# Kernel tuning notes

Hardware: AMD Instinct MI355X
Metric: run time of the kernel (lower is better)

Reference implementation:

```python
import jax, jax.numpy as jnp
import numpy as np


def _hardswish(x):
    return x * jnp.clip(x + 3.0, 0.0, 6.0) / 6.0


def _rel_coords_table(W):
    # [1, 2W-1, 2W-1, 2], log-spaced continuous relative coords (SwinV2)
    rc = jnp.arange(-(W - 1), W, dtype=jnp.float32)
    grid = jnp.stack(jnp.meshgrid(rc, rc, indexing='ij'), axis=-1)[None]
    grid = grid / float(W - 1) * 8.0
    return jnp.sign(grid) * jnp.log2(jnp.abs(grid) + 1.0) / np.float32(np.log2(8.0))


def _rel_pos_index(W):
    # [N, N] int indices into the (2W-1)^2 bias table
    coords = np.stack(np.meshgrid(np.arange(W), np.arange(W), indexing='ij')).reshape(2, -1)
    rel = (coords[:, :, None] - coords[:, None, :]).transpose(1, 2, 0)  # [N, N, 2]
    rel[:, :, 0] += W - 1
    rel[:, :, 1] += W - 1
    rel[:, :, 0] *= 2 * W - 1
    return jnp.asarray(rel.sum(-1))


def setup_inputs() -> dict:
    key = jax.random.key(0)
    ks = jax.random.split(key, 6)
    dim, num_heads, W = 512, 16, 8
    N = W * W
    B, nW = 2048, 64
    return {
        'x': jax.random.normal(ks[0], (B, N, dim), jnp.float32),
        'mask': jax.random.normal(ks[1], (nW, N, N), jnp.float32),
        'w_qkv': jax.random.normal(ks[2], (dim, 3 * dim), jnp.float32) * 0.02,
        'w_out': jax.random.normal(ks[3], (dim, dim), jnp.float32) * 0.02,
        'cpb_w1': jax.random.normal(ks[4], (2, 512), jnp.float32) * 0.02,
        'cpb_w2': jax.random.normal(ks[5], (512, num_heads), jnp.float32) * 0.02,
        'logits_scale': jnp.log(10.0 * jnp.ones((num_heads, 1, 1), jnp.float32)),
        'window_size': W,
        'num_heads': num_heads,
    }


def reference(x, mask, w_qkv, w_out, cpb_w1, cpb_w2, logits_scale, window_size, num_heads):
    B, N, C = x.shape
    hd = C // num_heads
    qkv = (x @ w_qkv).reshape(B, N, 3, num_heads, hd).transpose(2, 0, 3, 1, 4)
    q, k, v = qkv[0], qkv[1], qkv[2]  # [B, H, N, hd]

    # cosine attention (L2-normalized q, k) with clamped learned logit scale
    qn = q / jnp.clip(jnp.linalg.norm(q, axis=-1, keepdims=True), 1e-12)
    kn = k / jnp.clip(jnp.linalg.norm(k, axis=-1, keepdims=True), 1e-12)
    attn = jnp.einsum('bhnd,bhmd->bhnm', qn, kn)
    scale = jnp.exp(jnp.minimum(logits_scale, jnp.log(jnp.float32(100.0))))  # [H,1,1]
    attn = attn * scale[None]

    # continuous position bias via tiny MLP + index gather, sigmoid-scaled
    table = _rel_coords_table(window_size)                       # [1, 2W-1, 2W-1, 2]
    bias_table = (_hardswish(table @ cpb_w1) @ cpb_w2).reshape(-1, num_heads)
    idx = _rel_pos_index(window_size)                            # [N, N]
    bias = bias_table[idx.reshape(-1)].reshape(N, N, num_heads).transpose(2, 0, 1)
    attn = attn + 16.0 * jax.nn.sigmoid(bias)[None]

    if mask is not None:
        nW = mask.shape[0]
        attn = attn.reshape(B // nW, nW, num_heads, N, N) + mask[None, :, None]
        attn = attn.reshape(B, num_heads, N, N)

    # NOTE: original uses nn.Softmax(1) -> softmax over the HEAD axis; replicate faithfully
    attn = jax.nn.softmax(attn, axis=1)

    out = jnp.einsum('bhnm,bhmd->bhnd', attn, v).transpose(0, 2, 1, 3).reshape(B, N, C)
    return out @ w_out
```

## Files before the change

kernel.cpp:

```cpp
#include <hip/hip_runtime.h>
#include <hip/hip_bf16.h>

typedef unsigned short u16;
typedef unsigned int u32;
typedef __attribute__((ext_vector_type(8))) short bf16x8;
typedef __attribute__((ext_vector_type(4))) float f32x4;
typedef __attribute__((ext_vector_type(4))) float float4v;

__device__ __forceinline__ float bf2f(u16 v) {
  union { u32 u; float f; } x; x.u = ((u32)v) << 16; return x.f;
}
__device__ __forceinline__ u16 f2bf(float f) {
  union { u32 u; float f; } x; x.f = f;
  return (u16)((x.u + 0x7fffu + ((x.u >> 16) & 1u)) >> 16);
}

__device__ __forceinline__ void gload16(const void* g, void* l) {
  __builtin_amdgcn_global_load_lds(
      (const __attribute__((address_space(1))) u32*)g,
      (__attribute__((address_space(3))) u32*)l, 16, 0, 0);
}

#define MFMA16(a, bfr, cacc) __builtin_amdgcn_mfma_f32_16x16x32_bf16((a), (bfr), (cacc), 0, 0, 0)


__global__ void transpose_kernel(const float* __restrict__ in, u16* __restrict__ out,
                                 int R, int C) {
  int t = blockIdx.x * blockDim.x + threadIdx.x;
  if (t >= R * C) return;
  int c = t / R, r = t % R;
  out[t] = f2bf(in[r * C + c]);
}

__global__ void bias_tab_kernel(const float* __restrict__ w1, const float* __restrict__ w2,
                                float* __restrict__ tab) {
  int t = blockIdx.x * blockDim.x + threadIdx.x;
  if (t >= 225 * 16) return;
  int r = t >> 4, h = t & 15;
  int i = r / 15, j = r % 15;
  float gi = (float)(i - 7) * (8.0f / 7.0f);
  float gj = (float)(j - 7) * (8.0f / 7.0f);
  float si = (gi > 0.f) ? 1.f : ((gi < 0.f) ? -1.f : 0.f);
  float sj = (gj > 0.f) ? 1.f : ((gj < 0.f) ? -1.f : 0.f);
  float t0 = si * log2f(fabsf(gi) + 1.0f) * (1.0f / 3.0f);
  float t1 = sj * log2f(fabsf(gj) + 1.0f) * (1.0f / 3.0f);
  float acc = 0.f;
  for (int k = 0; k < 512; ++k) {
    float a = t0 * w1[k] + t1 * w1[512 + k];
    float hs = a * fminf(fmaxf(a + 3.f, 0.f), 6.f) * (1.f / 6.f);
    acc += hs * w2[k * 16 + h];
  }
  tab[t] = acc;
}

__global__ void bias16_kernel(const float* __restrict__ tab, float* __restrict__ b16) {
  int t = blockIdx.x * blockDim.x + threadIdx.x;
  if (t >= 16 * 64 * 64) return;
  int h = t >> 12, nm = t & 4095, n = nm >> 6, m = nm & 63;
  int idx = ((n >> 3) - (m >> 3) + 7) * 15 + ((n & 7) - (m & 7) + 7);
  float b = tab[idx * 16 + h];
  b16[t] = 16.0f / (1.0f + expf(-b));
}

template <bool F32OUT>
__global__ __launch_bounds__(256) void gemm_bt(const u16* __restrict__ A,
                                               const u16* __restrict__ Bt,
                                               void* __restrict__ Cout,
                                               int M, int N, int K) {
  __shared__ u16 lA[128 * 64];
  __shared__ u16 lB[128 * 64];
  const int tid = threadIdx.x;
  const int w = tid >> 6, l = tid & 63;
  const int lg = l >> 4, li = l & 15;
  const int nbn = N >> 7;
  const int nwg = gridDim.x;
  int bidx = blockIdx.x;
  int q = nwg >> 3, r = nwg & 7;
  int xcd = bidx & 7, pos = bidx >> 3;
  int swz = (xcd < r ? xcd * (q + 1) : r * (q + 1) + (xcd - r) * q) + pos;
  int bm = swz / nbn, bn = swz % nbn;
  const int wr = w >> 1, wc = w & 1;

  f32x4 acc[4][4];
#pragma unroll
  for (int i = 0; i < 4; i++)
#pragma unroll
    for (int j = 0; j < 4; j++) acc[i][j] = (f32x4){0.f, 0.f, 0.f, 0.f};

  const u16* Abase = A + (size_t)(bm * 128) * K;
  const u16* Bbase = Bt + (size_t)(bn * 128) * K;

  for (int k0 = 0; k0 < K; k0 += 64) {
#pragma unroll
    for (int i = 0; i < 4; ++i) {
      int c = w * 256 + i * 64 + l;
      int row = c >> 3, kc = c & 7;
      gload16(Abase + (size_t)row * K + k0 + kc * 8, (u16*)lA + c * 8);
      gload16(Bbase + (size_t)row * K + k0 + kc * 8, (u16*)lB + c * 8);
    }
    __syncthreads();
#pragma unroll
    for (int kk = 0; kk < 2; ++kk) {
      bf16x8 af[4], bfr[4];
#pragma unroll
      for (int t = 0; t < 4; ++t) {
        int row = wr * 64 + t * 16 + li;
        af[t] = *(const bf16x8*)&lA[row * 64 + kk * 32 + lg * 8];
        int col = wc * 64 + t * 16 + li;
        bfr[t] = *(const bf16x8*)&lB[col * 64 + kk * 32 + lg * 8];
      }
#pragma unroll
      for (int tm = 0; tm < 4; ++tm)
#pragma unroll
        for (int tn = 0; tn < 4; ++tn)
          acc[tm][tn] = MFMA16(af[tm], bfr[tn], acc[tm][tn]);
    }
    __syncthreads();
  }
  int r0 = bm * 128 + wr * 64 + lg * 4;
  int c0 = bn * 128 + wc * 64 + li;
#pragma unroll
  for (int tm = 0; tm < 4; ++tm)
#pragma unroll
    for (int tn = 0; tn < 4; ++tn)
#pragma unroll
      for (int j = 0; j < 4; ++j) {
        size_t off = (size_t)(r0 + tm * 16 + j) * N + c0 + tn * 16;
        if (F32OUT)
          ((float*)Cout)[off] = acc[tm][tn][j];
        else
          ((u16*)Cout)[off] = f2bf(acc[tm][tn][j]);
      }
}

__global__ __launch_bounds__(1024, 4) void fused_attn(const float* __restrict__ x,
                                                      const float* __restrict__ mask,
                                                      const u16* __restrict__ wqkvT,
                                                      const float* __restrict__ bias16,
                                                      const float* __restrict__ lscale,
                                                      u16* __restrict__ aout) {
  __shared__ float S[16 * 32 * 65];
  u16* xl = (u16*)S;
  u16* bb = xl + 32768;
  float* ob = S;

  const int tid = threadIdx.x;
  const int h = tid >> 6, l = tid & 63;
  const int lg = l >> 4, li = l & 15;
  const int b = blockIdx.x, wm = b & 63;
  const float* xg = x + (size_t)b * 64 * 512;

  {
    int n = tid >> 4, seg = tid & 15;
    const float4v* src = (const float4v*)(xg + n * 512 + seg * 32);
#pragma unroll
    for (int i = 0; i < 4; ++i) {
      float4v a = src[2 * i], c = src[2 * i + 1];
      union { bf16x8 v; u16 s[8]; } o;
      o.s[0] = f2bf(a[0]); o.s[1] = f2bf(a[1]); o.s[2] = f2bf(a[2]); o.s[3] = f2bf(a[3]);
      o.s[4] = f2bf(c[0]); o.s[5] = f2bf(c[1]); o.s[6] = f2bf(c[2]); o.s[7] = f2bf(c[3]);
      *(bf16x8*)(xl + ((n * 64 + ((seg * 4 + i) ^ (n & 7))) << 3)) = o.v;
    }
  }
  float sc = __expf(fminf(lscale[h], 4.6051702f));
  __syncthreads();

  bf16x8 qf[4], kf[4];

  {
    f32x4 qa[4][2], ka[4][2];
#pragma unroll
    for (int rt = 0; rt < 4; ++rt)
#pragma unroll
      for (int dt = 0; dt < 2; ++dt) {
        qa[rt][dt] = (f32x4){0.f, 0.f, 0.f, 0.f};
        ka[rt][dt] = (f32x4){0.f, 0.f, 0.f, 0.f};
      }
    const u16* bqp = wqkvT + (size_t)(h * 32) * 512;
    const u16* bkp = wqkvT + (size_t)(512 + h * 32) * 512;
#pragma unroll
    for (int kk = 0; kk < 16; ++kk) {
      bf16x8 ax[4];
#pragma unroll
      for (int rt = 0; rt < 4; ++rt) {
        int n = rt * 16 + li;
        ax[rt] = *(const bf16x8*)(xl + ((n * 64 + ((kk * 4 + lg) ^ (n & 7))) << 3));
      }
#pragma unroll
      for (int dt = 0; dt < 2; ++dt) {
        int coff = (dt * 16 + li) * 512 + kk * 32 + lg * 8;
        bf16x8 fq = *(const bf16x8*)(bqp + coff);
        bf16x8 fk = *(const bf16x8*)(bkp + coff);
#pragma unroll
        for (int rt = 0; rt < 4; ++rt) {
          qa[rt][dt] = MFMA16(ax[rt], fq, qa[rt][dt]);
          ka[rt][dt] = MFMA16(ax[rt], fk, ka[rt][dt]);
        }
      }
    }
    f32x4 rqs[4], rks[4];
#pragma unroll
    for (int rt = 0; rt < 4; ++rt) {
      f32x4 q2, k2;
#pragma unroll
      for (int j = 0; j < 4; ++j) {
        q2[j] = qa[rt][0][j] * qa[rt][0][j] + qa[rt][1][j] * qa[rt][1][j];
        k2[j] = ka[rt][0][j] * ka[rt][0][j] + ka[rt][1][j] * ka[rt][1][j];
      }
#pragma unroll
      for (int s = 1; s <= 8; s <<= 1)
#pragma unroll
        for (int j = 0; j < 4; ++j) {
          q2[j] += __shfl_xor(q2[j], s);
          k2[j] += __shfl_xor(k2[j], s);
        }
#pragma unroll
      for (int j = 0; j < 4; ++j) {
        rqs[rt][j] = sc / fmaxf(sqrtf(q2[j]), 1e-12f);
        rks[rt][j] = 1.0f / fmaxf(sqrtf(k2[j]), 1e-12f);
      }
    }
#pragma unroll
    for (int rt = 0; rt < 4; ++rt)
#pragma unroll
      for (int dt = 0; dt < 2; ++dt)
#pragma unroll
        for (int j = 0; j < 4; ++j) {
          int n = rt * 16 + lg * 4 + j;
          int d = dt * 16 + li;
          int s = (n ^ (n >> 2)) & 3;
          bb[h * 2048 + n * 32 + (((d >> 3) ^ s) << 3) + (d & 7)] =
              f2bf(qa[rt][dt][j] * rqs[rt][j]);
        }
    __syncthreads();
#pragma unroll
    for (int t = 0; t < 4; ++t) {
      int n = t * 16 + li;
      int s = (n ^ (n >> 2)) & 3;
      qf[t] = *(const bf16x8*)(bb + h * 2048 + n * 32 + ((lg ^ s) << 3));
    }
    __syncthreads();
#pragma unroll
    for (int rt = 0; rt < 4; ++rt)
#pragma unroll
      for (int dt = 0; dt < 2; ++dt)
#pragma unroll
        for (int j = 0; j < 4; ++j) {
          int n = rt * 16 + lg * 4 + j;
          int d = dt * 16 + li;
          int s = (n ^ (n >> 2)) & 3;
          bb[h * 2048 + n * 32 + (((d >> 3) ^ s) << 3) + (d & 7)] =
              f2bf(ka[rt][dt][j] * rks[rt][j]);
        }
    __syncthreads();
#pragma unroll
    for (int t = 0; t < 4; ++t) {
      int n = t * 16 + li;
      int s = (n ^ (n >> 2)) & 3;
      kf[t] = *(const bf16x8*)(bb + h * 2048 + n * 32 + ((lg ^ s) << 3));
    }
  }

  f32x4 va[4][2];
#pragma unroll
  for (int rt = 0; rt < 4; ++rt)
#pragma unroll
    for (int dt = 0; dt < 2; ++dt) va[rt][dt] = (f32x4){0.f, 0.f, 0.f, 0.f};
  {
    const u16* bvp = wqkvT + (size_t)(1024 + h * 32) * 512;
#pragma unroll
    for (int kk = 0; kk < 16; ++kk) {
      bf16x8 ax[4];
#pragma unroll
      for (int rt = 0; rt < 4; ++rt) {
        int n = rt * 16 + li;
        ax[rt] = *(const bf16x8*)(xl + ((n * 64 + ((kk * 4 + lg) ^ (n & 7))) << 3));
      }
#pragma unroll
      for (int dt = 0; dt < 2; ++dt) {
        bf16x8 fv = *(const bf16x8*)(bvp + (dt * 16 + li) * 512 + kk * 32 + lg * 8);
#pragma unroll
        for (int rt = 0; rt < 4; ++rt) va[rt][dt] = MFMA16(ax[rt], fv, va[rt][dt]);
      }
    }
  }
  __syncthreads();

  const float* bias_h = bias16 + h * 4096;
  const float* mask_w = mask + wm * 4096;
  f32x4 oacc[4][2];
#pragma unroll
  for (int i = 0; i < 4; i++) {
    oacc[i][0] = (f32x4){0.f, 0.f, 0.f, 0.f};
    oacc[i][1] = (f32x4){0.f, 0.f, 0.f, 0.f};
  }

#pragma unroll
  for (int c = 0; c < 2; ++c) {
#pragma unroll
    for (int tn = 0; tn < 4; ++tn)
#pragma unroll
      for (int t = 0; t < 2; ++t) {
        int mt = c * 2 + t;
        f32x4 z = {0.f, 0.f, 0.f, 0.f};
        f32x4 s = MFMA16(qf[tn], kf[mt], z);
        int mloc = t * 16 + li;
        int mg = c * 32 + mloc;
#pragma unroll
        for (int j = 0; j < 4; ++j) {
          int n = tn * 16 + lg * 4 + j;
          S[h * 2080 + mloc * 65 + n] = s[j] + bias_h[n * 64 + mg] + mask_w[n * 64 + mg];
        }
      }
    __syncthreads();
#pragma unroll
    for (int pp = 0; pp < 2; ++pp) {
      int p = tid + pp * 1024;
      int base = (p >> 6) * 65 + (p & 63);
      float vals[16];
      float mx = -3.0e38f;
#pragma unroll
      for (int hh = 0; hh < 16; ++hh) {
        vals[hh] = S[hh * 2080 + base];
        mx = fmaxf(mx, vals[hh]);
      }
      float sum = 0.f;
#pragma unroll
      for (int hh = 0; hh < 16; ++hh) {
        float e = __expf(vals[hh] - mx);
        vals[hh] = e;
        sum += e;
      }
      float inv = 1.0f / sum;
#pragma unroll
      for (int hh = 0; hh < 16; ++hh) S[hh * 2080 + base] = vals[hh] * inv;
    }
    __syncthreads();
    bf16x8 vf[2];
#pragma unroll
    for (int td = 0; td < 2; ++td)
#pragma unroll
      for (int j = 0; j < 8; ++j) {
        int srcl = (((lg * 2 + (j >> 2)) & 3) << 4) + li;
        float a0 = __shfl(va[c * 2][td][j & 3], srcl);
        float a1 = __shfl(va[c * 2 + 1][td][j & 3], srcl);
        vf[td][j] = (short)f2bf(lg >= 2 ? a1 : a0);
      }
#pragma unroll
    for (int tn = 0; tn < 4; ++tn) {
      bf16x8 pf;
#pragma unroll
      for (int j = 0; j < 8; ++j)
        pf[j] = (short)f2bf(S[h * 2080 + (lg * 8 + j) * 65 + tn * 16 + li]);
      oacc[tn][0] = MFMA16(pf, vf[0], oacc[tn][0]);
      oacc[tn][1] = MFMA16(pf, vf[1], oacc[tn][1]);
    }
    __syncthreads();
  }

#pragma unroll
  for (int tn = 0; tn < 4; ++tn)
#pragma unroll
    for (int td = 0; td < 2; ++td)
#pragma unroll
      for (int j = 0; j < 4; ++j) {
        int n = tn * 16 + lg * 4 + j;
        ob[n * 516 + h * 32 + td * 16 + li] = oacc[tn][td][j];
      }
  __syncthreads();
  {
    int n = tid >> 4, seg = tid & 15;
    u16* dst = aout + ((size_t)b * 64 + n) * 512 + seg * 32;
    const float* srcr = ob + n * 516 + seg * 32;
#pragma unroll
    for (int i = 0; i < 4; ++i) {
      union { bf16x8 v; u16 s[8]; } o;
#pragma unroll
      for (int e = 0; e < 8; ++e) o.s[e] = f2bf(srcr[i * 8 + e]);
      *(bf16x8*)(dst + i * 8) = o.v;
    }
  }
}

extern "C" void kernel_launch(void* const* d_in, const int* in_sizes, int n_in,
                              void* d_out, int out_size, void* d_ws, size_t ws_size,
                              hipStream_t stream) {
  const float* x = (const float*)d_in[0];
  const float* mask = (const float*)d_in[1];
  const float* w_qkv = (const float*)d_in[2];
  const float* w_out = (const float*)d_in[3];
  const float* cpb_w1 = (const float*)d_in[4];
  const float* cpb_w2 = (const float*)d_in[5];
  const float* lscale = (const float*)d_in[6];
  float* out = (float*)d_out;

  char* ws = (char*)d_ws;
  u16* wqkvT = (u16*)ws;
  u16* woutT = (u16*)(ws + 1572864ull);
  float* btab = (float*)(ws + 2097152ull);
  float* b16 = (float*)(ws + 2113536ull);
  u16* attn_out = (u16*)(ws + 2375680ull);

  transpose_kernel<<<(512 * 1536 + 255) / 256, 256, 0, stream>>>(w_qkv, wqkvT, 512, 1536);
  transpose_kernel<<<(512 * 512 + 255) / 256, 256, 0, stream>>>(w_out, woutT, 512, 512);
  bias_tab_kernel<<<(225 * 16 + 255) / 256, 256, 0, stream>>>(cpb_w1, cpb_w2, btab);
  bias16_kernel<<<(16 * 64 * 64 + 255) / 256, 256, 0, stream>>>(btab, b16);

  fused_attn<<<2048, 1024, 0, stream>>>(x, mask, wqkvT, b16, lscale, attn_out);

  gemm_bt<true><<<4096, 256, 0, stream>>>(attn_out, woutT, out, 131072, 512, 512);
}
```

Measured before the change: 956.9 us.

## Stage V in LDS, shrink score buffer with 16-column chunks, fold norms into accumulators

V is now written to LDS as bf16 after its projection instead of staying in registers for shuffles, which frees the va accumulators. The attention loop now processes four chunks of 16 key columns instead of two of 32. This halves the S score buffer, and each thread runs a single softmax over heads per chunk. The norm scales are applied in place to the q and k accumulators. The aim is to lower register and LDS pressure, but the PV MFMAs now zero half their K dimension, the loop needs more barriers, and more MFMAs are issued.

```diff
diff --git a/kernel.cpp b/kernel.cpp
--- a/kernel.cpp
+++ b/kernel.cpp
@@ -139,9 +139,10 @@
                                                       const float* __restrict__ bias16,
                                                       const float* __restrict__ lscale,
                                                       u16* __restrict__ aout) {
-  __shared__ float S[16 * 32 * 65];
+  __shared__ float S[34048];
   u16* xl = (u16*)S;
   u16* bb = xl + 32768;
+  u16* vl = xl + 33280;
   float* ob = S;
 
   const int tid = threadIdx.x;
@@ -198,7 +199,6 @@
         }
       }
     }
-    f32x4 rqs[4], rks[4];
 #pragma unroll
     for (int rt = 0; rt < 4; ++rt) {
       f32x4 q2, k2;
@@ -216,8 +216,13 @@
         }
 #pragma unroll
       for (int j = 0; j < 4; ++j) {
-        rqs[rt][j] = sc / fmaxf(sqrtf(q2[j]), 1e-12f);
-        rks[rt][j] = 1.0f / fmaxf(sqrtf(k2[j]), 1e-12f);
+        float rq = sc / fmaxf(sqrtf(q2[j]), 1e-12f);
+        float rk = 1.0f / fmaxf(sqrtf(k2[j]), 1e-12f);
+#pragma unroll
+        for (int dt = 0; dt < 2; ++dt) {
+          qa[rt][dt][j] *= rq;
+          ka[rt][dt][j] *= rk;
+        }
       }
     }
 #pragma unroll
@@ -229,8 +234,7 @@
           int n = rt * 16 + lg * 4 + j;
           int d = dt * 16 + li;
           int s = (n ^ (n >> 2)) & 3;
-          bb[h * 2048 + n * 32 + (((d >> 3) ^ s) << 3) + (d & 7)] =
-              f2bf(qa[rt][dt][j] * rqs[rt][j]);
+          bb[h * 2048 + n * 32 + (((d >> 3) ^ s) << 3) + (d & 7)] = f2bf(qa[rt][dt][j]);
         }
     __syncthreads();
 #pragma unroll
@@ -249,8 +253,7 @@
           int n = rt * 16 + lg * 4 + j;
           int d = dt * 16 + li;
           int s = (n ^ (n >> 2)) & 3;
-          bb[h * 2048 + n * 32 + (((d >> 3) ^ s) << 3) + (d & 7)] =
-              f2bf(ka[rt][dt][j] * rks[rt][j]);
+          bb[h * 2048 + n * 32 + (((d >> 3) ^ s) << 3) + (d & 7)] = f2bf(ka[rt][dt][j]);
         }
     __syncthreads();
 #pragma unroll
@@ -260,13 +263,14 @@
       kf[t] = *(const bf16x8*)(bb + h * 2048 + n * 32 + ((lg ^ s) << 3));
     }
   }
-
-  f32x4 va[4][2];
-#pragma unroll
-  for (int rt = 0; rt < 4; ++rt)
-#pragma unroll
-    for (int dt = 0; dt < 2; ++dt) va[rt][dt] = (f32x4){0.f, 0.f, 0.f, 0.f};
+  __syncthreads();
+
   {
+    f32x4 va[4][2];
+#pragma unroll
+    for (int rt = 0; rt < 4; ++rt)
+#pragma unroll
+      for (int dt = 0; dt < 2; ++dt) va[rt][dt] = (f32x4){0.f, 0.f, 0.f, 0.f};
     const u16* bvp = wqkvT + (size_t)(1024 + h * 32) * 512;
 #pragma unroll
     for (int kk = 0; kk < 16; ++kk) {
@@ -283,11 +287,22 @@
         for (int rt = 0; rt < 4; ++rt) va[rt][dt] = MFMA16(ax[rt], fv, va[rt][dt]);
       }
     }
+    u16* vh = vl + h * 2176;
+#pragma unroll
+    for (int rt = 0; rt < 4; ++rt)
+#pragma unroll
+      for (int dt = 0; dt < 2; ++dt)
+#pragma unroll
+        for (int j = 0; j < 4; ++j) {
+          int m = rt * 16 + lg * 4 + j;
+          vh[m * 34 + dt * 16 + li] = f2bf(va[rt][dt][j]);
+        }
   }
   __syncthreads();
 
   const float* bias_h = bias16 + h * 4096;
   const float* mask_w = mask + wm * 4096;
+  const u16* vh = vl + h * 2176;
   f32x4 oacc[4][2];
 #pragma unroll
   for (int i = 0; i < 4; i++) {
@@ -296,32 +311,26 @@
   }
 
 #pragma unroll
-  for (int c = 0; c < 2; ++c) {
-#pragma unroll
-    for (int tn = 0; tn < 4; ++tn)
-#pragma unroll
-      for (int t = 0; t < 2; ++t) {
-        int mt = c * 2 + t;
-        f32x4 z = {0.f, 0.f, 0.f, 0.f};
-        f32x4 s = MFMA16(qf[tn], kf[mt], z);
-        int mloc = t * 16 + li;
-        int mg = c * 32 + mloc;
-#pragma unroll
-        for (int j = 0; j < 4; ++j) {
-          int n = tn * 16 + lg * 4 + j;
-          S[h * 2080 + mloc * 65 + n] = s[j] + bias_h[n * 64 + mg] + mask_w[n * 64 + mg];
-        }
-      }
-    __syncthreads();
-#pragma unroll
-    for (int pp = 0; pp < 2; ++pp) {
-      int p = tid + pp * 1024;
-      int base = (p >> 6) * 65 + (p & 63);
+  for (int c = 0; c < 4; ++c) {
+#pragma unroll
+    for (int tn = 0; tn < 4; ++tn) {
+      f32x4 z = {0.f, 0.f, 0.f, 0.f};
+      f32x4 s = MFMA16(qf[tn], kf[c], z);
+      int mg = c * 16 + li;
+#pragma unroll
+      for (int j = 0; j < 4; ++j) {
+        int n = tn * 16 + lg * 4 + j;
+        S[h * 1040 + li * 65 + n] = s[j] + bias_h[n * 64 + mg] + mask_w[n * 64 + mg];
+      }
+    }
+    __syncthreads();
+    {
+      int base = (tid >> 6) * 65 + (tid & 63);
       float vals[16];
       float mx = -3.0e38f;
 #pragma unroll
       for (int hh = 0; hh < 16; ++hh) {
-        vals[hh] = S[hh * 2080 + base];
+        vals[hh] = S[hh * 1040 + base];
         mx = fmaxf(mx, vals[hh]);
       }
       float sum = 0.f;
@@ -333,27 +342,25 @@
       }
       float inv = 1.0f / sum;
 #pragma unroll
-      for (int hh = 0; hh < 16; ++hh) S[hh * 2080 + base] = vals[hh] * inv;
-    }
-    __syncthreads();
-    bf16x8 vf[2];
-#pragma unroll
-    for (int td = 0; td < 2; ++td)
-#pragma unroll
-      for (int j = 0; j < 8; ++j) {
-        int srcl = (((lg * 2 + (j >> 2)) & 3) << 4) + li;
-        float a0 = __shfl(va[c * 2][td][j & 3], srcl);
-        float a1 = __shfl(va[c * 2 + 1][td][j & 3], srcl);
-        vf[td][j] = (short)f2bf(lg >= 2 ? a1 : a0);
-      }
-#pragma unroll
-    for (int tn = 0; tn < 4; ++tn) {
-      bf16x8 pf;
-#pragma unroll
-      for (int j = 0; j < 8; ++j)
-        pf[j] = (short)f2bf(S[h * 2080 + (lg * 8 + j) * 65 + tn * 16 + li]);
-      oacc[tn][0] = MFMA16(pf, vf[0], oacc[tn][0]);
-      oacc[tn][1] = MFMA16(pf, vf[1], oacc[tn][1]);
+      for (int hh = 0; hh < 16; ++hh) S[hh * 1040 + base] = vals[hh] * inv;
+    }
+    __syncthreads();
+#pragma unroll
+    for (int td = 0; td < 2; ++td) {
+      bf16x8 vf;
+#pragma unroll
+      for (int e = 0; e < 8; ++e)
+        vf[e] = (lg < 2) ? (short)vh[(c * 16 + lg * 8 + e) * 34 + td * 16 + li]
+                         : (short)0;
+#pragma unroll
+      for (int tn = 0; tn < 4; ++tn) {
+        bf16x8 pf;
+#pragma unroll
+        for (int e = 0; e < 8; ++e)
+          pf[e] = (lg < 2) ? (short)f2bf(S[h * 1040 + (lg * 8 + e) * 65 + tn * 16 + li])
+                           : (short)0;
+        oacc[tn][td] = MFMA16(pf, vf, oacc[tn][td]);
+      }
     }
     __syncthreads();
   }
```

After: 1.054 ms. +10.2%, slower.

## Pre-swizzle QKV weights for coalesced fragment loads and cut register pressure in attention

Applied to the files above, without the earlier changes.

Replaces the plain QKV weight transpose with a swizzle kernel that stores weights in MFMA fragment order, so each wave's B-fragment load is a contiguous 1KB read instead of strided rows. Inside the fused kernel, the norm scaling is applied in place to the accumulators, the softmax no longer keeps a 16-entry register array, and the normalized probabilities are written as bf16 into LDS so the PV stage reads them without converting. It also switches the occupancy hint to waves_per_eu(4,4). These changes target global-load efficiency and register pressure, at the cost of extra LDS round-trips in the softmax.

```diff
diff --git a/kernel.cpp b/kernel.cpp
--- a/kernel.cpp
+++ b/kernel.cpp
@@ -30,6 +30,18 @@
   if (t >= R * C) return;
   int c = t / R, r = t % R;
   out[t] = f2bf(in[r * C + c]);
+}
+
+__global__ void wqkv_swz_kernel(const float* __restrict__ w, u16* __restrict__ out) {
+  int t = blockIdx.x * blockDim.x + threadIdx.x;
+  if (t >= 48 * 16384) return;
+  int whead = t >> 14;
+  int rest = t & 16383;
+  int chunk = rest >> 7;
+  int kk = chunk >> 3, dt = (chunk >> 2) & 1, lg = chunk & 3;
+  int li = (rest >> 3) & 15, e = rest & 7;
+  int s = whead >> 4, h = whead & 15;
+  out[t] = f2bf(w[(size_t)(kk * 32 + lg * 8 + e) * 1536 + s * 512 + h * 32 + dt * 16 + li]);
 }
 
 __global__ void bias_tab_kernel(const float* __restrict__ w1, const float* __restrict__ w2,
@@ -133,16 +145,16 @@
       }
 }
 
-__global__ __launch_bounds__(1024, 4) void fused_attn(const float* __restrict__ x,
-                                                      const float* __restrict__ mask,
-                                                      const u16* __restrict__ wqkvT,
-                                                      const float* __restrict__ bias16,
-                                                      const float* __restrict__ lscale,
-                                                      u16* __restrict__ aout) {
-  __shared__ float S[16 * 32 * 65];
+__global__ __launch_bounds__(1024)
+__attribute__((amdgpu_waves_per_eu(4, 4))) void fused_attn(
+    const float* __restrict__ x, const float* __restrict__ mask,
+    const u16* __restrict__ wqkv2, const float* __restrict__ bias16,
+    const float* __restrict__ lscale, u16* __restrict__ aout) {
+  __shared__ float S[33280];
   u16* xl = (u16*)S;
   u16* bb = xl + 32768;
   float* ob = S;
+  u16* P16 = (u16*)S;
 
   const int tid = threadIdx.x;
   const int h = tid >> 6, l = tid & 63;
@@ -176,8 +188,8 @@
         qa[rt][dt] = (f32x4){0.f, 0.f, 0.f, 0.f};
         ka[rt][dt] = (f32x4){0.f, 0.f, 0.f, 0.f};
       }
-    const u16* bqp = wqkvT + (size_t)(h * 32) * 512;
-    const u16* bkp = wqkvT + (size_t)(512 + h * 32) * 512;
+    const u16* bq2 = wqkv2 + (size_t)h * 16384;
+    const u16* bk2 = wqkv2 + (size_t)(16 + h) * 16384;
 #pragma unroll
     for (int kk = 0; kk < 16; ++kk) {
       bf16x8 ax[4];
@@ -188,9 +200,9 @@
       }
 #pragma unroll
       for (int dt = 0; dt < 2; ++dt) {
-        int coff = (dt * 16 + li) * 512 + kk * 32 + lg * 8;
-        bf16x8 fq = *(const bf16x8*)(bqp + coff);
-        bf16x8 fk = *(const bf16x8*)(bkp + coff);
+        int coff = (kk * 2 + dt) * 512 + lg * 128 + li * 8;
+        bf16x8 fq = *(const bf16x8*)(bq2 + coff);
+        bf16x8 fk = *(const bf16x8*)(bk2 + coff);
 #pragma unroll
         for (int rt = 0; rt < 4; ++rt) {
           qa[rt][dt] = MFMA16(ax[rt], fq, qa[rt][dt]);
@@ -198,7 +210,6 @@
         }
       }
     }
-    f32x4 rqs[4], rks[4];
 #pragma unroll
     for (int rt = 0; rt < 4; ++rt) {
       f32x4 q2, k2;
@@ -216,8 +227,13 @@
         }
 #pragma unroll
       for (int j = 0; j < 4; ++j) {
-        rqs[rt][j] = sc / fmaxf(sqrtf(q2[j]), 1e-12f);
-        rks[rt][j] = 1.0f / fmaxf(sqrtf(k2[j]), 1e-12f);
+        float rq = sc / fmaxf(sqrtf(q2[j]), 1e-12f);
+        float rk = 1.0f / fmaxf(sqrtf(k2[j]), 1e-12f);
+#pragma unroll
+        for (int dt = 0; dt < 2; ++dt) {
+          qa[rt][dt][j] *= rq;
+          ka[rt][dt][j] *= rk;
+        }
       }
     }
 #pragma unroll
@@ -229,8 +245,7 @@
           int n = rt * 16 + lg * 4 + j;
           int d = dt * 16 + li;
           int s = (n ^ (n >> 2)) & 3;
-          bb[h * 2048 + n * 32 + (((d >> 3) ^ s) << 3) + (d & 7)] =
-              f2bf(qa[rt][dt][j] * rqs[rt][j]);
+          bb[h * 2048 + n * 32 + (((d >> 3) ^ s) << 3) + (d & 7)] = f2bf(qa[rt][dt][j]);
         }
     __syncthreads();
 #pragma unroll
@@ -249,8 +264,7 @@
           int n = rt * 16 + lg * 4 + j;
           int d = dt * 16 + li;
           int s = (n ^ (n >> 2)) & 3;
-          bb[h * 2048 + n * 32 + (((d >> 3) ^ s) << 3) + (d & 7)] =
-              f2bf(ka[rt][dt][j] * rks[rt][j]);
+          bb[h * 2048 + n * 32 + (((d >> 3) ^ s) << 3) + (d & 7)] = f2bf(ka[rt][dt][j]);
         }
     __syncthreads();
 #pragma unroll
@@ -267,7 +281,7 @@
 #pragma unroll
     for (int dt = 0; dt < 2; ++dt) va[rt][dt] = (f32x4){0.f, 0.f, 0.f, 0.f};
   {
-    const u16* bvp = wqkvT + (size_t)(1024 + h * 32) * 512;
+    const u16* bv2 = wqkv2 + (size_t)(32 + h) * 16384;
 #pragma unroll
     for (int kk = 0; kk < 16; ++kk) {
       bf16x8 ax[4];
@@ -278,7 +292,7 @@
       }
 #pragma unroll
       for (int dt = 0; dt < 2; ++dt) {
-        bf16x8 fv = *(const bf16x8*)(bvp + (dt * 16 + li) * 512 + kk * 32 + lg * 8);
+        bf16x8 fv = *(const bf16x8*)(bv2 + (kk * 2 + dt) * 512 + lg * 128 + li * 8);
 #pragma unroll
         for (int rt = 0; rt < 4; ++rt) va[rt][dt] = MFMA16(ax[rt], fv, va[rt][dt]);
       }
@@ -317,23 +331,20 @@
     for (int pp = 0; pp < 2; ++pp) {
       int p = tid + pp * 1024;
       int base = (p >> 6) * 65 + (p & 63);
-      float vals[16];
       float mx = -3.0e38f;
 #pragma unroll
+      for (int hh = 0; hh < 16; ++hh) mx = fmaxf(mx, S[hh * 2080 + base]);
+      float sum = 0.f;
+#pragma unroll
       for (int hh = 0; hh < 16; ++hh) {
-        vals[hh] = S[hh * 2080 + base];
-        mx = fmaxf(mx, vals[hh]);
-      }
-      float sum = 0.f;
-#pragma unroll
-      for (int hh = 0; hh < 16; ++hh) {
-        float e = __expf(vals[hh] - mx);
-        vals[hh] = e;
+        float e = __expf(S[hh * 2080 + base] - mx);
+        S[hh * 2080 + base] = e;
         sum += e;
       }
       float inv = 1.0f / sum;
 #pragma unroll
-      for (int hh = 0; hh < 16; ++hh) S[hh * 2080 + base] = vals[hh] * inv;
+      for (int hh = 0; hh < 16; ++hh)
+        P16[(hh * 2080 + base) * 2] = f2bf(S[hh * 2080 + base] * inv);
     }
     __syncthreads();
     bf16x8 vf[2];
@@ -350,8 +361,8 @@
     for (int tn = 0; tn < 4; ++tn) {
       bf16x8 pf;
 #pragma unroll
-      for (int j = 0; j < 8; ++j)
-        pf[j] = (short)f2bf(S[h * 2080 + (lg * 8 + j) * 65 + tn * 16 + li]);
+      for (int e = 0; e < 8; ++e)
+        pf[e] = (short)P16[(h * 2080 + (lg * 8 + e) * 65 + tn * 16 + li) * 2];
       oacc[tn][0] = MFMA16(pf, vf[0], oacc[tn][0]);
       oacc[tn][1] = MFMA16(pf, vf[1], oacc[tn][1]);
     }
@@ -395,18 +406,18 @@
   float* out = (float*)d_out;
 
   char* ws = (char*)d_ws;
-  u16* wqkvT = (u16*)ws;
+  u16* wqkv2 = (u16*)ws;
   u16* woutT = (u16*)(ws + 1572864ull);
   float* btab = (float*)(ws + 2097152ull);
   float* b16 = (float*)(ws + 2113536ull);
   u16* attn_out = (u16*)(ws + 2375680ull);
 
-  transpose_kernel<<<(512 * 1536 + 255) / 256, 256, 0, stream>>>(w_qkv, wqkvT, 512, 1536);
+  wqkv_swz_kernel<<<(48 * 16384) / 256, 256, 0, stream>>>(w_qkv, wqkv2);
   transpose_kernel<<<(512 * 512 + 255) / 256, 256, 0, stream>>>(w_out, woutT, 512, 512);
   bias_tab_kernel<<<(225 * 16 + 255) / 256, 256, 0, stream>>>(cpb_w1, cpb_w2, btab);
   bias16_kernel<<<(16 * 64 * 64 + 255) / 256, 256, 0, stream>>>(btab, b16);
 
-  fused_attn<<<2048, 1024, 0, stream>>>(x, mask, wqkvT, b16, lscale, attn_out);
+  fused_attn<<<2048, 1024, 0, stream>>>(x, mask, wqkv2, b16, lscale, attn_out);
 
   gemm_bt<true><<<4096, 256, 0, stream>>>(attn_out, woutT, out, 131072, 512, 512);
 }
```

Result: no change. 942.6 us (-1.5%).
